# Kernel optimization log

Hardware: AMD Instinct MI355X
Metric: run time of the kernel (lower is better)

Reference implementation:

```python
import jax, jax.numpy as jnp
import numpy as np

B, S, H = 1, 2048, 2048
HD, NQ, NKV = 128, 16, 4
FFH = 8192
EPS = 1e-5
ROPE_BASE = 10000.0
SOFTMAX_CAP = 50.0
CLIP_L, CLIP_R = 0.0, 1.0


def setup_inputs() -> dict:
    key = jax.random.key(0)
    ks = jax.random.split(key, 10)
    std = 0.02
    return {
        "x": jax.random.normal(ks[0], (B, S, H), dtype=jnp.float32),
        "attn_norm_w": jax.random.uniform(ks[1], (H,), minval=-1.0, maxval=1.0, dtype=jnp.float32),
        "mlp_norm_w": jax.random.uniform(ks[2], (H,), minval=-1.0, maxval=1.0, dtype=jnp.float32),
        "wq": jax.random.normal(ks[3], (H, NQ * HD), dtype=jnp.float32) * std,
        "wk": jax.random.normal(ks[4], (H, NKV * HD), dtype=jnp.float32) * std,
        "wv": jax.random.normal(ks[5], (H, NKV * HD), dtype=jnp.float32) * std,
        "wo": jax.random.normal(ks[6], (NQ * HD, H), dtype=jnp.float32) * std,
        "w_gate": jax.random.normal(ks[7], (H, FFH), dtype=jnp.float32) * std,
        "w_up": jax.random.normal(ks[8], (H, FFH), dtype=jnp.float32) * std,
        "w_down": jax.random.normal(ks[9], (FFH, H), dtype=jnp.float32) * std,
    }


def _rms_norm(x, w):
    # GroupRMSNorm with group_size=None -> whole hidden dim
    var = jnp.mean(jnp.square(x), axis=-1, keepdims=True)
    return x * jax.lax.rsqrt(var + EPS) * w


def _rope_cos_sin(seq_len, dim):
    inv_freq = 1.0 / (ROPE_BASE ** (jnp.arange(0, dim, 2, dtype=jnp.float32) / dim))
    t = jnp.arange(seq_len, dtype=jnp.float32)
    freqs = jnp.outer(t, inv_freq)                      # [S, dim/2]
    emb = jnp.concatenate([freqs, freqs], axis=-1)      # [S, dim]
    return jnp.cos(emb), jnp.sin(emb)


def _apply_rope(x, cos, sin):
    # x: [B, S, h, d]; rotate-half (LLaMA-style)
    d = x.shape[-1]
    x1, x2 = x[..., : d // 2], x[..., d // 2 :]
    rot = jnp.concatenate([-x2, x1], axis=-1)
    return x * cos[None, :, None, :] + rot * sin[None, :, None, :]


def _qk_norm(x):
    # per-head RMS norm over head_dim (qk_norm_group_size == head_dim), unit weight
    var = jnp.mean(jnp.square(x), axis=-1, keepdims=True)
    return x * jax.lax.rsqrt(var + EPS)


def reference(x, attn_norm_w, mlp_norm_w, wq, wk, wv, wo, w_gate, w_up, w_down):
    # ---- attention sub-layer ----
    h = _rms_norm(x, attn_norm_w)                                     # [B,S,H]
    q = (h @ wq).reshape(B, S, NQ, HD)
    k = (h @ wk).reshape(B, S, NKV, HD)
    v = (h @ wv).reshape(B, S, NKV, HD)

    cos, sin = _rope_cos_sin(S, HD)
    q = _apply_rope(q, cos, sin)
    k = _apply_rope(k, cos, sin)

    q = _qk_norm(q)
    k = _qk_norm(k)

    # GQA: expand kv heads to match q heads
    rep = NQ // NKV
    k = jnp.repeat(k, rep, axis=2)                                    # [B,S,NQ,HD]
    v = jnp.repeat(v, rep, axis=2)

    scale = 1.0 / jnp.sqrt(jnp.float32(HD))
    scores = jnp.einsum("bshd,bthd->bhst", q, k) * scale              # [B,NQ,S,S]
    # softmax cap: cap * tanh(s / cap)
    scores = SOFTMAX_CAP * jnp.tanh(scores / SOFTMAX_CAP)
    causal = jnp.tril(jnp.ones((S, S), dtype=bool))
    scores = jnp.where(causal[None, None], scores, -jnp.inf)
    p = jax.nn.softmax(scores, axis=-1)
    # clip range (l, r): clamp(p * (r - l) + l, 0, 1)
    p = jnp.clip(p * (CLIP_R - CLIP_L) + CLIP_L, 0.0, 1.0)
    o = jnp.einsum("bhst,bthd->bshd", p, v).reshape(B, S, NQ * HD)
    x = x + o @ wo

    # ---- MLP sub-layer (gated SiLU) ----
    h2 = _rms_norm(x, mlp_norm_w)
    mlp_out = (jax.nn.silu(h2 @ w_gate) * (h2 @ w_up)) @ w_down
    return x + mlp_out
```

## Files before the change

### kernel.cpp

```cpp
#include <hip/hip_runtime.h>

typedef __bf16 bf16;
typedef __bf16 bf16x4 __attribute__((ext_vector_type(4)));
typedef __bf16 bf16x8 __attribute__((ext_vector_type(8)));
typedef float f32x4 __attribute__((ext_vector_type(4)));

#define GLP16(gp, lp) __builtin_amdgcn_global_load_lds( \
    (const __attribute__((address_space(1))) void*)(gp), \
    (__attribute__((address_space(3))) void*)(lp), 16, 0, 0)

__device__ __forceinline__ f32x4 mfma16(bf16x8 a, bf16x8 b, f32x4 c) {
    return __builtin_amdgcn_mfma_f32_16x16x32_bf16(a, b, c, 0, 0, 0);
}

__global__ __launch_bounds__(256) void k_rmsnorm(const float* __restrict__ x,
        const float* __restrict__ w, bf16* __restrict__ out) {
    const int H = 2048;
    size_t row = blockIdx.x;
    const float* xr = x + row * H;
    int base = threadIdx.x * 8;
    float4 a = *(const float4*)(xr + base);
    float4 b = *(const float4*)(xr + base + 4);
    float ss = a.x*a.x + a.y*a.y + a.z*a.z + a.w*a.w
             + b.x*b.x + b.y*b.y + b.z*b.z + b.w*b.w;
#pragma unroll
    for (int m = 32; m > 0; m >>= 1) ss += __shfl_xor(ss, m);
    __shared__ float red[4];
    if ((threadIdx.x & 63) == 0) red[threadIdx.x >> 6] = ss;
    __syncthreads();
    float tot = red[0] + red[1] + red[2] + red[3];
    float rs = rsqrtf(tot * (1.0f / H) + 1e-5f);
    float4 wa = *(const float4*)(w + base);
    float4 wb = *(const float4*)(w + base + 4);
    bf16x8 ov;
    ov[0] = (bf16)(a.x * rs * wa.x); ov[1] = (bf16)(a.y * rs * wa.y);
    ov[2] = (bf16)(a.z * rs * wa.z); ov[3] = (bf16)(a.w * rs * wa.w);
    ov[4] = (bf16)(b.x * rs * wb.x); ov[5] = (bf16)(b.y * rs * wb.y);
    ov[6] = (bf16)(b.z * rs * wb.z); ov[7] = (bf16)(b.w * rs * wb.w);
    *(bf16x8*)(out + row * H + base) = ov;
}

__global__ __launch_bounds__(256) void k_convT(const float* __restrict__ W,
        bf16* __restrict__ Wt, int K, int N, int rmul, int roff) {
    __shared__ float t[64][65];
    int k0 = blockIdx.x * 64, n0 = blockIdx.y * 64;
    int tid = threadIdx.x;
#pragma unroll
    for (int it = 0; it < 4; it++) {
        int idx = it * 256 + tid;
        int r = idx >> 4, c = (idx & 15) * 4;
        float4 v = *(const float4*)(W + (size_t)(k0 + r) * N + n0 + c);
        t[r][c] = v.x; t[r][c + 1] = v.y; t[r][c + 2] = v.z; t[r][c + 3] = v.w;
    }
    __syncthreads();
#pragma unroll
    for (int it = 0; it < 4; it++) {
        int idx = it * 256 + tid;
        int n = idx >> 4, kc = (idx & 15) * 4;
        bf16x4 o;
#pragma unroll
        for (int j = 0; j < 4; j++) o[j] = (bf16)t[kc + j][n];
        *(bf16x4*)(Wt + ((size_t)(n0 + n) * rmul + roff) * K + k0 + kc) = o;
    }
}

__global__ __launch_bounds__(256) void k_transpose(const bf16* __restrict__ in,
        bf16* __restrict__ out, int R, int C) {
    __shared__ bf16 t[32][33];
    int r0 = blockIdx.x * 32, c0 = blockIdx.y * 32;
    int tx = threadIdx.x & 31, ty = threadIdx.x >> 5;
#pragma unroll
    for (int i = 0; i < 4; i++)
        t[ty + i * 8][tx] = in[(size_t)(r0 + ty + i * 8) * C + c0 + tx];
    __syncthreads();
#pragma unroll
    for (int i = 0; i < 4; i++)
        out[(size_t)(c0 + ty + i * 8) * R + r0 + tx] = t[tx][ty + i * 8];
}

template<int EPI>
__global__ __launch_bounds__(512, 2) void k_gemm8(const bf16* __restrict__ A,
        const bf16* __restrict__ Bt, void* __restrict__ outp,
        const void* __restrict__ aux, int M, int N, int K, int ksplit) {
    extern __shared__ char lds[];
    const int tid = threadIdx.x, wave = tid >> 6, lane = tid & 63;
    const int lr = lane & 15, kg = lane >> 4;
    const int wm = wave >> 2, wn = wave & 3;
    const int bn = blockIdx.x, bm = blockIdx.y, split = blockIdx.z;
    const int row0 = bm * 256, col0 = bn * 256;
    const int kbeg = split * ksplit;
    const int NT = ksplit >> 6;
    const size_t K2 = (size_t)K * 2;
    const int xorm = (lr & 7) << 4;

    size_t soff[2];
#pragma unroll
    for (int s = 0; s < 2; s++) {
        int d = s * 8192 + tid * 16;
        int rh = d >> 7, c = d & 127;
        soff[s] = (size_t)rh * K2 + (c ^ ((rh & 7) << 4));
    }
    const char* Ab = (const char*)A + ((size_t)row0 * K + kbeg) * 2;
    const char* Bb = (const char*)Bt + ((size_t)col0 * K + kbeg) * 2;

    auto stA = [&](int t, int mh) {
        const char* src = Ab + (size_t)(mh * 128) * K2 + (size_t)t * 128;
        char* dst = lds + (t & 1) * 32768 + mh * 16384 + wave * 1024;
        GLP16(src + soff[0], dst);
        GLP16(src + soff[1], dst + 8192);
    };
    auto stB = [&](int t, int nh) {
        const char* src = Bb + (size_t)(nh * 128) * K2 + (size_t)t * 128;
        char* dst = lds + 65536 + (t & 1) * 32768 + nh * 16384 + wave * 1024;
        GLP16(src + soff[0], dst);
        GLP16(src + soff[1], dst + 8192);
    };

    f32x4 acc[8][4];
#pragma unroll
    for (int m = 0; m < 8; m++)
#pragma unroll
        for (int n = 0; n < 4; n++) acc[m][n] = (f32x4){0, 0, 0, 0};

    bf16x8 a[8], c0[4], c1[4];
    auto rdA = [&](const char* base, int mh) {
#pragma unroll
        for (int mi = 0; mi < 4; mi++)
#pragma unroll
            for (int kk = 0; kk < 2; kk++) {
                int rh = wm * 64 + mi * 16 + lr;
                int c = (kk * 64 + kg * 16) ^ xorm;
                a[mi * 2 + kk] = *(const bf16x8*)(base + mh * 16384 + rh * 128 + c);
            }
    };
    auto rdB = [&](const char* base, int nh, bf16x8 (&b)[4]) {
#pragma unroll
        for (int nj = 0; nj < 2; nj++)
#pragma unroll
            for (int kk = 0; kk < 2; kk++) {
                int rh = wn * 32 + nj * 16 + lr;
                int c = (kk * 64 + kg * 16) ^ xorm;
                b[nj * 2 + kk] = *(const bf16x8*)(base + nh * 16384 + rh * 128 + c);
            }
    };
    auto mm = [&](int mh, int nh, bf16x8 (&b)[4]) {
#pragma unroll
        for (int mi = 0; mi < 4; mi++)
#pragma unroll
            for (int nj = 0; nj < 2; nj++)
#pragma unroll
                for (int kk = 0; kk < 2; kk++)
                    acc[mh * 4 + mi][nh * 2 + nj] =
                        mfma16(a[mi * 2 + kk], b[nj * 2 + kk],
                               acc[mh * 4 + mi][nh * 2 + nj]);
    };

#define PBAR do { asm volatile("" ::: "memory"); \
                  __builtin_amdgcn_s_barrier(); \
                  asm volatile("" ::: "memory"); } while (0)

    stA(0, 0); stA(0, 1); stB(0, 0); stB(0, 1);
    asm volatile("s_waitcnt vmcnt(0)" ::: "memory");
    PBAR;

    for (int t = 0; t < NT; ++t) {
        const char* Ac = lds + (t & 1) * 32768;
        const char* Bc = lds + 65536 + (t & 1) * 32768;
        const bool m1 = (t + 1 < NT);
        rdA(Ac, 0); rdB(Bc, 0, c0); rdB(Bc, 1, c1);
        if (m1) { stA(t + 1, 0); stA(t + 1, 1); stB(t + 1, 0); stB(t + 1, 1); }
        __builtin_amdgcn_s_setprio(1);
        mm(0, 0, c0); mm(0, 1, c1);
        __builtin_amdgcn_s_setprio(0);
        PBAR;
        rdA(Ac, 1);
        __builtin_amdgcn_s_setprio(1);
        mm(1, 0, c0); mm(1, 1, c1);
        __builtin_amdgcn_s_setprio(0);
        if (m1) asm volatile("s_waitcnt vmcnt(0)" ::: "memory");
        PBAR;
    }
#undef PBAR

#pragma unroll
    for (int mi = 0; mi < 8; mi++)
#pragma unroll
        for (int ni = 0; ni < 4; ni++)
#pragma unroll
            for (int r = 0; r < 4; r++) {
                size_t row = row0 + (mi >> 2) * 128 + wm * 64 + (mi & 3) * 16 + kg * 4 + r;
                size_t col = col0 + (ni >> 1) * 128 + wn * 32 + (ni & 1) * 16 + lr;
                float vv = acc[mi][ni][r];
                if (EPI == 5) {
                    ((bf16*)outp)[(size_t)split * M * N + row * N + col] = (bf16)vv;
                } else {
                    float pv = __shfl_xor(vv, 1);
                    float g = (lane & 1) ? pv : vv;
                    float u = (lane & 1) ? vv : pv;
                    float sg = g / (1.0f + __expf(-g));
                    if (!(lane & 1))
                        ((bf16*)outp)[row * (size_t)(N >> 1) + (col >> 1)] =
                            (bf16)(sg * u);
                }
            }
}

__global__ __launch_bounds__(256) void k_reduce(const bf16* __restrict__ parts,
        const float* __restrict__ resid, float* __restrict__ out,
        int ns, size_t n8) {
    size_t i = (size_t)blockIdx.x * 256 + threadIdx.x;
    if (i >= n8) return;
    size_t base = i * 8;
    float4 a = *(const float4*)(resid + base);
    float4 b = *(const float4*)(resid + base + 4);
    for (int s = 0; s < ns; s++) {
        bf16x8 p = *(const bf16x8*)(parts + (size_t)s * n8 * 8 + base);
        a.x += (float)p[0]; a.y += (float)p[1]; a.z += (float)p[2]; a.w += (float)p[3];
        b.x += (float)p[4]; b.y += (float)p[5]; b.z += (float)p[6]; b.w += (float)p[7];
    }
    *(float4*)(out + base) = a;
    *(float4*)(out + base + 4) = b;
}

__global__ __launch_bounds__(256) void k_reduce_rms(const bf16* __restrict__ parts,
        const float* __restrict__ resid, const float* __restrict__ w,
        float* __restrict__ x2, bf16* __restrict__ hb, int ns) {
    const int H = 2048;
    size_t row = blockIdx.x;
    int base = threadIdx.x * 8;
    const float* rr = resid + row * H + base;
    float4 a = *(const float4*)rr;
    float4 b = *(const float4*)(rr + 4);
    for (int s = 0; s < ns; s++) {
        bf16x8 p = *(const bf16x8*)(parts + (size_t)s * H * 2048 + row * H + base);
        a.x += (float)p[0]; a.y += (float)p[1]; a.z += (float)p[2]; a.w += (float)p[3];
        b.x += (float)p[4]; b.y += (float)p[5]; b.z += (float)p[6]; b.w += (float)p[7];
    }
    *(float4*)(x2 + row * H + base) = a;
    *(float4*)(x2 + row * H + base + 4) = b;
    float ss = a.x*a.x + a.y*a.y + a.z*a.z + a.w*a.w
             + b.x*b.x + b.y*b.y + b.z*b.z + b.w*b.w;
#pragma unroll
    for (int m = 32; m > 0; m >>= 1) ss += __shfl_xor(ss, m);
    __shared__ float red[4];
    if ((threadIdx.x & 63) == 0) red[threadIdx.x >> 6] = ss;
    __syncthreads();
    float tot = red[0] + red[1] + red[2] + red[3];
    float rs = rsqrtf(tot * (1.0f / H) + 1e-5f);
    float4 wa = *(const float4*)(w + base);
    float4 wb = *(const float4*)(w + base + 4);
    bf16x8 ov;
    ov[0] = (bf16)(a.x * rs * wa.x); ov[1] = (bf16)(a.y * rs * wa.y);
    ov[2] = (bf16)(a.z * rs * wa.z); ov[3] = (bf16)(a.w * rs * wa.w);
    ov[4] = (bf16)(b.x * rs * wb.x); ov[5] = (bf16)(b.y * rs * wb.y);
    ov[6] = (bf16)(b.z * rs * wb.z); ov[7] = (bf16)(b.w * rs * wb.w);
    *(bf16x8*)(hb + row * H + base) = ov;
}

__global__ __launch_bounds__(256) void k_qkvrope(const bf16* __restrict__ parts,
        bf16* __restrict__ qb, bf16* __restrict__ kb, bf16* __restrict__ vb) {
    int s = blockIdx.x;
    int tid = threadIdx.x, wave = tid >> 6, lane = tid & 63;
    const bf16* p0 = parts + (size_t)s * 3072;
    const bf16* p1 = p0 + (size_t)2048 * 3072;
    float f = exp2f((float)lane * -0.2076205059304601f);
    float sn, cs;
    sincosf((float)s * f, &sn, &cs);
#pragma unroll 1
    for (int pass = 0; pass < 5; pass++) {
        int h = pass * 4 + wave;
        int base = (h < 16) ? h * 128 : 2048 + (h - 16) * 128;
        int c1 = base + lane, c2 = c1 + 64;
        float x1 = (float)p0[c1] + (float)p1[c1];
        float x2 = (float)p0[c2] + (float)p1[c2];
        float o1 = x1 * cs - x2 * sn;
        float o2 = x2 * cs + x1 * sn;
        float ss = o1 * o1 + o2 * o2;
#pragma unroll
        for (int m = 32; m > 0; m >>= 1) ss += __shfl_xor(ss, m);
        float rs = rsqrtf(ss * (1.0f / 128.0f) + 1e-5f);
        bf16* dst = (h < 16) ? (qb + (size_t)s * 2048 + h * 128)
                             : (kb + (size_t)s * 512 + (h - 16) * 128);
        dst[lane] = (bf16)(o1 * rs);
        dst[lane + 64] = (bf16)(o2 * rs);
    }
    int c = 2560 + tid * 2;
    float v0 = (float)p0[c] + (float)p1[c];
    float v1 = (float)p0[c + 1] + (float)p1[c + 1];
    bf16* vd = vb + (size_t)s * 512 + tid * 2;
    vd[0] = (bf16)v0; vd[1] = (bf16)v1;
}

__global__ __launch_bounds__(256, 2) void k_attn(const bf16* __restrict__ qg,
        const bf16* __restrict__ kgl, const bf16* __restrict__ vtg,
        bf16* __restrict__ og) {
    extern __shared__ char alds[];
    int pi = blockIdx.x, h = blockIdx.y, kvh = h >> 2;
    int qt = (pi & 1) ? (31 - (pi >> 1)) : (pi >> 1);
    int nt = qt + 1;
    int tid = threadIdx.x, wave = tid >> 6, lane = tid & 63;
    int lr = lane & 15, kgrp = lane >> 4;

    int rowQ[4], colQ[4], rowV[4], colV[4];
#pragma unroll
    for (int j = 0; j < 4; j++) {
        int p = j * 4096 + wave * 1024 + lane * 16;
        int ps = p ^ (((p >> 8) & 7) << 4);
        rowQ[j] = ps >> 8; colQ[j] = ps & 255;
        int pv = p ^ (((p >> 7) & 7) << 4);
        rowV[j] = pv >> 7; colV[j] = pv & 127;
    }

    const float C1 = 0.08838834764831845f / 50.0f;
    const float L2E50 = 72.13475204444817f;

#pragma unroll
    for (int j = 0; j < 4; j++)
        GLP16((const char*)qg + (size_t)(qt * 64 + rowQ[j]) * 4096 + h * 256 + colQ[j],
              alds + j * 4096 + wave * 1024);
    for (int t = 0; t < 2 && t < nt; t++) {
#pragma unroll
        for (int j = 0; j < 4; j++)
            GLP16((const char*)kgl + (size_t)(t * 64 + rowQ[j]) * 1024 + kvh * 256 + colQ[j],
                  alds + 16384 + t * 16384 + j * 4096 + wave * 1024);
#pragma unroll
        for (int j = 0; j < 4; j++)
            GLP16((const char*)vtg + (size_t)(kvh * 128 + rowV[j]) * 4096 + t * 128 + colV[j],
                  alds + 49152 + t * 16384 + j * 4096 + wave * 1024);
    }
    if (nt > 1) asm volatile("s_waitcnt vmcnt(8)" ::: "memory");
    else        asm volatile("s_waitcnt vmcnt(0)" ::: "memory");
    __builtin_amdgcn_s_barrier();

    bf16x8 qf[4];
#pragma unroll
    for (int c = 0; c < 4; c++) {
        int b = (wave * 16 + lr) * 256 + c * 64 + kgrp * 16;
        qf[c] = *(const bf16x8*)(alds + (b ^ (((b >> 8) & 7) << 4)));
    }
    __builtin_amdgcn_s_barrier();

    f32x4 accO[8];
#pragma unroll
    for (int n = 0; n < 8; n++) accO[n] = (f32x4){0, 0, 0, 0};
    float lsum[4] = {0, 0, 0, 0};
    int qrow = qt * 64 + wave * 16 + kgrp * 4;

    for (int kt = 0; kt < nt; kt++) {
        int buf = kt & 1;
        const char* Kb = alds + 16384 + buf * 16384;
        const char* Vb = alds + 49152 + buf * 16384;
        char* Pb = alds;
#pragma unroll
        for (int j = 0; j < 4; j++) {
            f32x4 s = {0, 0, 0, 0};
#pragma unroll
            for (int c = 0; c < 4; c++) {
                int b = (j * 16 + lr) * 256 + c * 64 + kgrp * 16;
                bf16x8 kf = *(const bf16x8*)(Kb + (b ^ (((b >> 8) & 7) << 4)));
                s = mfma16(qf[c], kf, s);
            }
            int key = kt * 64 + j * 16 + lr;
#pragma unroll
            for (int r = 0; r < 4; r++) {
                float y = s[r] * C1;
                float y2 = y * y;
                float u = fmaf(y2, 0.13333333f, -0.33333333f);
                u = fmaf(y2, u, 1.0f);
                float t5 = y * u;
                float pe = fmaf(t5, L2E50, -L2E50);
                float pv = (key <= qrow + r) ? exp2f(pe) : 0.0f;
                lsum[r] += pv;
                int wb = (wave * 16 + kgrp * 4 + r) * 128 + (j * 16 + lr) * 2;
                *(bf16*)(Pb + (wb ^ (((wb >> 7) & 7) << 4))) = (bf16)pv;
            }
        }
        bf16x8 pf[2];
#pragma unroll
        for (int ks2 = 0; ks2 < 2; ks2++) {
            int b = (wave * 16 + lr) * 128 + ks2 * 64 + kgrp * 16;
            pf[ks2] = *(const bf16x8*)(Pb + (b ^ (((b >> 7) & 7) << 4)));
        }
#pragma unroll
        for (int n = 0; n < 8; n++)
#pragma unroll
            for (int ks2 = 0; ks2 < 2; ks2++) {
                int b = (n * 16 + lr) * 128 + ks2 * 64 + kgrp * 16;
                bf16x8 vf = *(const bf16x8*)(Vb + (b ^ (((b >> 7) & 7) << 4)));
                accO[n] = mfma16(pf[ks2], vf, accO[n]);
            }
        __builtin_amdgcn_s_barrier();
        bool more = (kt + 2 < nt);
        if (more) {
            int t = kt + 2;
#pragma unroll
            for (int j = 0; j < 4; j++)
                GLP16((const char*)kgl + (size_t)(t * 64 + rowQ[j]) * 1024 + kvh * 256 + colQ[j],
                      alds + 16384 + buf * 16384 + j * 4096 + wave * 1024);
#pragma unroll
            for (int j = 0; j < 4; j++)
                GLP16((const char*)vtg + (size_t)(kvh * 128 + rowV[j]) * 4096 + t * 128 + colV[j],
                      alds + 49152 + buf * 16384 + j * 4096 + wave * 1024);
        }
        if (kt + 1 < nt) {
            if (more) asm volatile("s_waitcnt vmcnt(8)" ::: "memory");
            else      asm volatile("s_waitcnt vmcnt(0)" ::: "memory");
            __builtin_amdgcn_s_barrier();
        }
    }
#pragma unroll
    for (int r = 0; r < 4; r++) {
        float t = lsum[r];
        t += __shfl_xor(t, 1); t += __shfl_xor(t, 2);
        t += __shfl_xor(t, 4); t += __shfl_xor(t, 8);
        lsum[r] = t;
    }
#pragma unroll
    for (int n = 0; n < 8; n++)
#pragma unroll
        for (int r = 0; r < 4; r++) {
            size_t row = qt * 64 + wave * 16 + kgrp * 4 + r;
            og[row * 2048 + h * 128 + n * 16 + lr] = (bf16)(accO[n][r] / lsum[r]);
        }
}

extern "C" void kernel_launch(void* const* d_in, const int* in_sizes, int n_in,
                              void* d_out, int out_size, void* d_ws, size_t ws_size,
                              hipStream_t stream) {
    const float* x      = (const float*)d_in[0];
    const float* attn_w = (const float*)d_in[1];
    const float* mlp_w  = (const float*)d_in[2];
    const float* wq     = (const float*)d_in[3];
    const float* wk     = (const float*)d_in[4];
    const float* wv     = (const float*)d_in[5];
    const float* wo     = (const float*)d_in[6];
    const float* wgate  = (const float*)d_in[7];
    const float* wup    = (const float*)d_in[8];
    const float* wdown  = (const float*)d_in[9];
    float* out = (float*)d_out;
    char* ws = (char*)d_ws;

    const size_t MB = 1024 * 1024;
    bf16* Wqkv = (bf16*)(ws + 0);
    bf16* vt   = (bf16*)(ws + 0);
    bf16* pO   = (bf16*)(ws + 0);
    bf16* Wgu  = (bf16*)(ws + 0);
    bf16* pD   = (bf16*)(ws + 0);
    bf16* WoT  = (bf16*)(ws + 64 * MB);
    bf16* WdT  = (bf16*)(ws + 64 * MB);
    bf16* hb   = (bf16*)(ws + 96 * MB);
    bf16* qb   = (bf16*)(ws + 104 * MB);
    bf16* kb   = (bf16*)(ws + 112 * MB);
    bf16* vb   = (bf16*)(ws + 114 * MB);
    bf16* ob   = (bf16*)(ws + 116 * MB);
    float* x2  = (float*)(ws + 124 * MB);
    bf16* gb   = (bf16*)(ws + 140 * MB);
    bf16* pQ   = (bf16*)(ws + 172 * MB);

    const int LDS8 = 131072;
    hipFuncSetAttribute((const void*)&k_gemm8<4>,
        hipFuncAttributeMaxDynamicSharedMemorySize, LDS8);
    hipFuncSetAttribute((const void*)&k_gemm8<5>,
        hipFuncAttributeMaxDynamicSharedMemorySize, LDS8);
    const int LDSA = 81920;
    hipFuncSetAttribute((const void*)&k_attn,
        hipFuncAttributeMaxDynamicSharedMemorySize, LDSA);

    const size_t n8 = (size_t)2048 * 2048 / 8;

    k_rmsnorm<<<2048, 256, 0, stream>>>(x, attn_w, hb);
    k_convT<<<dim3(32, 32), 256, 0, stream>>>(wq, Wqkv, 2048, 2048, 1, 0);
    k_convT<<<dim3(32, 8), 256, 0, stream>>>(wk, Wqkv + 4194304, 2048, 512, 1, 0);
    k_convT<<<dim3(32, 8), 256, 0, stream>>>(wv, Wqkv + 5242880, 2048, 512, 1, 0);
    k_gemm8<5><<<dim3(12, 8, 2), 512, LDS8, stream>>>(hb, Wqkv, pQ, nullptr,
                                                      2048, 3072, 2048, 1024);
    k_qkvrope<<<2048, 256, 0, stream>>>(pQ, qb, kb, vb);
    k_transpose<<<dim3(64, 16), 256, 0, stream>>>(vb, vt, 2048, 512);
    k_attn<<<dim3(32, 16), 256, LDSA, stream>>>(qb, kb, vt, ob);
    k_convT<<<dim3(32, 32), 256, 0, stream>>>(wo, WoT, 2048, 2048, 1, 0);
    k_gemm8<5><<<dim3(8, 8, 4), 512, LDS8, stream>>>(ob, WoT, pO, nullptr,
                                                     2048, 2048, 2048, 512);
    k_reduce_rms<<<2048, 256, 0, stream>>>(pO, x, mlp_w, x2, hb, 4);
    k_convT<<<dim3(32, 128), 256, 0, stream>>>(wgate, Wgu, 2048, 8192, 2, 0);
    k_convT<<<dim3(32, 128), 256, 0, stream>>>(wup, Wgu, 2048, 8192, 2, 1);
    k_gemm8<4><<<dim3(64, 8, 1), 512, LDS8, stream>>>(hb, Wgu, gb, nullptr,
                                                      2048, 16384, 2048, 2048);
    k_convT<<<dim3(128, 32), 256, 0, stream>>>(wdown, WdT, 8192, 2048, 1, 0);
    k_gemm8<5><<<dim3(8, 8, 4), 512, LDS8, stream>>>(gb, WdT, pD, nullptr,
                                                     2048, 2048, 8192, 2048);
    k_reduce<<<2048, 256, 0, stream>>>(pD, x2, out, 4, n8);
}
```

Measured before the change: 438.2 us.

## Shrink GEMM tile to 256x128 with BK=32, two-stage prefetch, higher occupancy

Replaces the 256x256x64 GEMM with a 256x128 tile, K-step 32, and an 8-wave 4x2 layout in which each wave owns a 64x64 sub-tile. It prefetches two stages ahead using vmcnt-based waits. LDS use drops to 48KB and launch bounds now request 4 blocks per CU, with twice as many blocks in every GEMM launch. The aim is better latency hiding through occupancy and deeper prefetch, at the cost of less operand reuse per block and more barriers per unit of K.

Result: slower. 473.3 us (+8.0%).

```diff
diff --git a/kernel.cpp b/kernel.cpp
--- a/kernel.cpp
+++ b/kernel.cpp
@@ -79,118 +79,111 @@
 }
 
 template<int EPI>
-__global__ __launch_bounds__(512, 2) void k_gemm8(const bf16* __restrict__ A,
+__global__ __launch_bounds__(512, 4) void k_gemm9(const bf16* __restrict__ A,
         const bf16* __restrict__ Bt, void* __restrict__ outp,
         const void* __restrict__ aux, int M, int N, int K, int ksplit) {
     extern __shared__ char lds[];
     const int tid = threadIdx.x, wave = tid >> 6, lane = tid & 63;
     const int lr = lane & 15, kg = lane >> 4;
-    const int wm = wave >> 2, wn = wave & 3;
+    const int wm = wave >> 1, wn = wave & 1;
     const int bn = blockIdx.x, bm = blockIdx.y, split = blockIdx.z;
-    const int row0 = bm * 256, col0 = bn * 256;
+    const int row0 = bm * 256, col0 = bn * 128;
     const int kbeg = split * ksplit;
-    const int NT = ksplit >> 6;
+    const int NT = ksplit >> 5;
     const size_t K2 = (size_t)K * 2;
-    const int xorm = (lr & 7) << 4;
-
-    size_t soff[2];
-#pragma unroll
-    for (int s = 0; s < 2; s++) {
-        int d = s * 8192 + tid * 16;
-        int rh = d >> 7, c = d & 127;
-        soff[s] = (size_t)rh * K2 + (c ^ ((rh & 7) << 4));
+
+    int soffA[2], soffB;
+    {
+#pragma unroll
+        for (int s = 0; s < 2; s++) {
+            int d = wave * 2048 + s * 1024 + lane * 16;
+            int line = d >> 7, w = d & 127;
+            int wp = w ^ ((line & 7) << 4);
+            soffA[s] = (line * 2 + (wp >> 6)) * (int)K2 + (wp & 63);
+        }
+        int d = wave * 1024 + lane * 16;
+        int line = d >> 7, w = d & 127;
+        int wp = w ^ ((line & 7) << 4);
+        soffB = (line * 2 + (wp >> 6)) * (int)K2 + (wp & 63);
     }
     const char* Ab = (const char*)A + ((size_t)row0 * K + kbeg) * 2;
     const char* Bb = (const char*)Bt + ((size_t)col0 * K + kbeg) * 2;
 
-    auto stA = [&](int t, int mh) {
-        const char* src = Ab + (size_t)(mh * 128) * K2 + (size_t)t * 128;
-        char* dst = lds + (t & 1) * 32768 + mh * 16384 + wave * 1024;
-        GLP16(src + soff[0], dst);
-        GLP16(src + soff[1], dst + 8192);
+    auto stage = [&](int t) {
+        const char* sa = Ab + (size_t)t * 64;
+        char* da = lds + (t & 1) * 16384 + wave * 2048;
+        GLP16(sa + soffA[0], da);
+        GLP16(sa + soffA[1], da + 1024);
+        const char* sb = Bb + (size_t)t * 64;
+        char* db = lds + 32768 + (t & 1) * 8192 + wave * 1024;
+        GLP16(sb + soffB, db);
     };
-    auto stB = [&](int t, int nh) {
-        const char* src = Bb + (size_t)(nh * 128) * K2 + (size_t)t * 128;
-        char* dst = lds + 65536 + (t & 1) * 32768 + nh * 16384 + wave * 1024;
-        GLP16(src + soff[0], dst);
-        GLP16(src + soff[1], dst + 8192);
+
+    f32x4 acc[4][4];
+#pragma unroll
+    for (int m = 0; m < 4; m++)
+#pragma unroll
+        for (int n = 0; n < 4; n++) acc[m][n] = (f32x4){0, 0, 0, 0};
+
+    bf16x8 a[4], b[4];
+    auto rdA = [&](const char* base) {
+#pragma unroll
+        for (int mi = 0; mi < 4; mi++) {
+            int r = wm * 64 + mi * 16 + lr;
+            int line = r >> 1;
+            int off = (((r & 1) << 6) + (kg << 4)) ^ ((line & 7) << 4);
+            a[mi] = *(const bf16x8*)(base + line * 128 + off);
+        }
     };
-
-    f32x4 acc[8][4];
-#pragma unroll
-    for (int m = 0; m < 8; m++)
-#pragma unroll
-        for (int n = 0; n < 4; n++) acc[m][n] = (f32x4){0, 0, 0, 0};
-
-    bf16x8 a[8], c0[4], c1[4];
-    auto rdA = [&](const char* base, int mh) {
+    auto rdB = [&](const char* base) {
+#pragma unroll
+        for (int nj = 0; nj < 4; nj++) {
+            int r = wn * 64 + nj * 16 + lr;
+            int line = r >> 1;
+            int off = (((r & 1) << 6) + (kg << 4)) ^ ((line & 7) << 4);
+            b[nj] = *(const bf16x8*)(base + line * 128 + off);
+        }
+    };
+    auto mm2 = [&](int njb) {
 #pragma unroll
         for (int mi = 0; mi < 4; mi++)
 #pragma unroll
-            for (int kk = 0; kk < 2; kk++) {
-                int rh = wm * 64 + mi * 16 + lr;
-                int c = (kk * 64 + kg * 16) ^ xorm;
-                a[mi * 2 + kk] = *(const bf16x8*)(base + mh * 16384 + rh * 128 + c);
-            }
-    };
-    auto rdB = [&](const char* base, int nh, bf16x8 (&b)[4]) {
-#pragma unroll
-        for (int nj = 0; nj < 2; nj++)
-#pragma unroll
-            for (int kk = 0; kk < 2; kk++) {
-                int rh = wn * 32 + nj * 16 + lr;
-                int c = (kk * 64 + kg * 16) ^ xorm;
-                b[nj * 2 + kk] = *(const bf16x8*)(base + nh * 16384 + rh * 128 + c);
-            }
-    };
-    auto mm = [&](int mh, int nh, bf16x8 (&b)[4]) {
-#pragma unroll
-        for (int mi = 0; mi < 4; mi++)
-#pragma unroll
-            for (int nj = 0; nj < 2; nj++)
-#pragma unroll
-                for (int kk = 0; kk < 2; kk++)
-                    acc[mh * 4 + mi][nh * 2 + nj] =
-                        mfma16(a[mi * 2 + kk], b[nj * 2 + kk],
-                               acc[mh * 4 + mi][nh * 2 + nj]);
+            for (int dn = 0; dn < 2; dn++)
+                acc[mi][njb + dn] = mfma16(a[mi], b[njb + dn], acc[mi][njb + dn]);
     };
 
 #define PBAR do { asm volatile("" ::: "memory"); \
                   __builtin_amdgcn_s_barrier(); \
                   asm volatile("" ::: "memory"); } while (0)
 
-    stA(0, 0); stA(0, 1); stB(0, 0); stB(0, 1);
-    asm volatile("s_waitcnt vmcnt(0)" ::: "memory");
+    stage(0); stage(1);
+    asm volatile("s_waitcnt vmcnt(3)" ::: "memory");
     PBAR;
 
-    for (int t = 0; t < NT; ++t) {
-        const char* Ac = lds + (t & 1) * 32768;
-        const char* Bc = lds + 65536 + (t & 1) * 32768;
-        const bool m1 = (t + 1 < NT);
-        rdA(Ac, 0); rdB(Bc, 0, c0); rdB(Bc, 1, c1);
-        if (m1) { stA(t + 1, 0); stA(t + 1, 1); stB(t + 1, 0); stB(t + 1, 1); }
-        __builtin_amdgcn_s_setprio(1);
-        mm(0, 0, c0); mm(0, 1, c1);
-        __builtin_amdgcn_s_setprio(0);
+    for (int s = 0; s < NT; ++s) {
+        const char* Ac = lds + (s & 1) * 16384;
+        const char* Bc = lds + 32768 + (s & 1) * 8192;
+        rdA(Ac); rdB(Bc);
+        __builtin_amdgcn_s_setprio(1); mm2(0); __builtin_amdgcn_s_setprio(0);
+        asm volatile("s_waitcnt lgkmcnt(0)" ::: "memory");
         PBAR;
-        rdA(Ac, 1);
-        __builtin_amdgcn_s_setprio(1);
-        mm(1, 0, c0); mm(1, 1, c1);
-        __builtin_amdgcn_s_setprio(0);
-        if (m1) asm volatile("s_waitcnt vmcnt(0)" ::: "memory");
+        if (s + 2 < NT) stage(s + 2);
+        __builtin_amdgcn_s_setprio(1); mm2(2); __builtin_amdgcn_s_setprio(0);
+        if (s + 2 < NT)      asm volatile("s_waitcnt vmcnt(3)" ::: "memory");
+        else if (s + 1 < NT) asm volatile("s_waitcnt vmcnt(0)" ::: "memory");
         PBAR;
     }
 #undef PBAR
 
 #pragma unroll
-    for (int mi = 0; mi < 8; mi++)
-#pragma unroll
-        for (int ni = 0; ni < 4; ni++)
+    for (int mi = 0; mi < 4; mi++)
+#pragma unroll
+        for (int nj = 0; nj < 4; nj++)
 #pragma unroll
             for (int r = 0; r < 4; r++) {
-                size_t row = row0 + (mi >> 2) * 128 + wm * 64 + (mi & 3) * 16 + kg * 4 + r;
-                size_t col = col0 + (ni >> 1) * 128 + wn * 32 + (ni & 1) * 16 + lr;
-                float vv = acc[mi][ni][r];
+                size_t row = row0 + wm * 64 + mi * 16 + kg * 4 + r;
+                size_t col = col0 + wn * 64 + nj * 16 + lr;
+                float vv = acc[mi][nj][r];
                 if (EPI == 5) {
                     ((bf16*)outp)[(size_t)split * M * N + row * N + col] = (bf16)vv;
                 } else {
@@ -457,11 +450,11 @@
     bf16* gb   = (bf16*)(ws + 140 * MB);
     bf16* pQ   = (bf16*)(ws + 172 * MB);
 
-    const int LDS8 = 131072;
-    hipFuncSetAttribute((const void*)&k_gemm8<4>,
-        hipFuncAttributeMaxDynamicSharedMemorySize, LDS8);
-    hipFuncSetAttribute((const void*)&k_gemm8<5>,
-        hipFuncAttributeMaxDynamicSharedMemorySize, LDS8);
+    const int LDS9 = 49152;
+    hipFuncSetAttribute((const void*)&k_gemm9<4>,
+        hipFuncAttributeMaxDynamicSharedMemorySize, LDS9);
+    hipFuncSetAttribute((const void*)&k_gemm9<5>,
+        hipFuncAttributeMaxDynamicSharedMemorySize, LDS9);
     const int LDSA = 81920;
     hipFuncSetAttribute((const void*)&k_attn,
         hipFuncAttributeMaxDynamicSharedMemorySize, LDSA);
@@ -472,21 +465,21 @@
     k_convT<<<dim3(32, 32), 256, 0, stream>>>(wq, Wqkv, 2048, 2048, 1, 0);
     k_convT<<<dim3(32, 8), 256, 0, stream>>>(wk, Wqkv + 4194304, 2048, 512, 1, 0);
     k_convT<<<dim3(32, 8), 256, 0, stream>>>(wv, Wqkv + 5242880, 2048, 512, 1, 0);
-    k_gemm8<5><<<dim3(12, 8, 2), 512, LDS8, stream>>>(hb, Wqkv, pQ, nullptr,
+    k_gemm9<5><<<dim3(24, 8, 2), 512, LDS9, stream>>>(hb, Wqkv, pQ, nullptr,
                                                       2048, 3072, 2048, 1024);
     k_qkvrope<<<2048, 256, 0, stream>>>(pQ, qb, kb, vb);
     k_transpose<<<dim3(64, 16), 256, 0, stream>>>(vb, vt, 2048, 512);
     k_attn<<<dim3(32, 16), 256, LDSA, stream>>>(qb, kb, vt, ob);
     k_convT<<<dim3(32, 32), 256, 0, stream>>>(wo, WoT, 2048, 2048, 1, 0);
-    k_gemm8<5><<<dim3(8, 8, 4), 512, LDS8, stream>>>(ob, WoT, pO, nullptr,
-                                                     2048, 2048, 2048, 512);
+    k_gemm9<5><<<dim3(16, 8, 4), 512, LDS9, stream>>>(ob, WoT, pO, nullptr,
+                                                      2048, 2048, 2048, 512);
     k_reduce_rms<<<2048, 256, 0, stream>>>(pO, x, mlp_w, x2, hb, 4);
     k_convT<<<dim3(32, 128), 256, 0, stream>>>(wgate, Wgu, 2048, 8192, 2, 0);
     k_convT<<<dim3(32, 128), 256, 0, stream>>>(wup, Wgu, 2048, 8192, 2, 1);
-    k_gemm8<4><<<dim3(64, 8, 1), 512, LDS8, stream>>>(hb, Wgu, gb, nullptr,
-                                                      2048, 16384, 2048, 2048);
+    k_gemm9<4><<<dim3(128, 8, 1), 512, LDS9, stream>>>(hb, Wgu, gb, nullptr,
+                                                       2048, 16384, 2048, 2048);
     k_convT<<<dim3(128, 32), 256, 0, stream>>>(wdown, WdT, 8192, 2048, 1, 0);
-    k_gemm8<5><<<dim3(8, 8, 4), 512, LDS8, stream>>>(gb, WdT, pD, nullptr,
-                                                     2048, 2048, 8192, 2048);
+    k_gemm9<5><<<dim3(16, 8, 4), 512, LDS9, stream>>>(gb, WdT, pD, nullptr,
+                                                      2048, 2048, 8192, 2048);
     k_reduce<<<2048, 256, 0, stream>>>(pD, x2, out, 4, n8);
 }
```

## Switch GEMM inner loop to 32x32x16 MFMA with per-wave 128x64 tiles

Applied to the files above, without the earlier changes.

The GEMM kernel now uses 32x32x16 bf16 MFMA instructions instead of 16x16x32. Each wave computes a 128x64 sub-tile instead of two 64x32 halves, and the LDS read pattern, staging loop and epilogue index mapping are rewritten to match. The larger MFMA shape issues fewer instructions and does fewer LDS fragment reads per FLOP. In exchange, register pressure and accumulator layout change, and the epilogue's SiLU pairing now depends on the new lane-to-column mapping.

Result: slower. 463.1 us (+5.7%).

```diff
diff --git a/kernel.cpp b/kernel.cpp
--- a/kernel.cpp
+++ b/kernel.cpp
@@ -4,6 +4,7 @@
 typedef __bf16 bf16x4 __attribute__((ext_vector_type(4)));
 typedef __bf16 bf16x8 __attribute__((ext_vector_type(8)));
 typedef float f32x4 __attribute__((ext_vector_type(4)));
+typedef float f32x16 __attribute__((ext_vector_type(16)));
 
 #define GLP16(gp, lp) __builtin_amdgcn_global_load_lds( \
     (const __attribute__((address_space(1))) void*)(gp), \
@@ -11,6 +12,9 @@
 
 __device__ __forceinline__ f32x4 mfma16(bf16x8 a, bf16x8 b, f32x4 c) {
     return __builtin_amdgcn_mfma_f32_16x16x32_bf16(a, b, c, 0, 0, 0);
+}
+__device__ __forceinline__ f32x16 mfma32(bf16x8 a, bf16x8 b, f32x16 c) {
+    return __builtin_amdgcn_mfma_f32_32x32x16_bf16(a, b, c, 0, 0, 0);
 }
 
 __global__ __launch_bounds__(256) void k_rmsnorm(const float* __restrict__ x,
@@ -79,87 +83,76 @@
 }
 
 template<int EPI>
-__global__ __launch_bounds__(512, 2) void k_gemm8(const bf16* __restrict__ A,
+__global__ __launch_bounds__(512, 2) void k_gemm10(const bf16* __restrict__ A,
         const bf16* __restrict__ Bt, void* __restrict__ outp,
         const void* __restrict__ aux, int M, int N, int K, int ksplit) {
     extern __shared__ char lds[];
     const int tid = threadIdx.x, wave = tid >> 6, lane = tid & 63;
-    const int lr = lane & 15, kg = lane >> 4;
+    const int l31 = lane & 31, lh = lane >> 5;
     const int wm = wave >> 2, wn = wave & 3;
     const int bn = blockIdx.x, bm = blockIdx.y, split = blockIdx.z;
     const int row0 = bm * 256, col0 = bn * 256;
     const int kbeg = split * ksplit;
     const int NT = ksplit >> 6;
     const size_t K2 = (size_t)K * 2;
-    const int xorm = (lr & 7) << 4;
-
-    size_t soff[2];
-#pragma unroll
-    for (int s = 0; s < 2; s++) {
-        int d = s * 8192 + tid * 16;
-        int rh = d >> 7, c = d & 127;
-        soff[s] = (size_t)rh * K2 + (c ^ ((rh & 7) << 4));
+
+    int soff[4];
+#pragma unroll
+    for (int c = 0; c < 4; c++) {
+        int d = c * 8192 + tid * 16;
+        int rh = d >> 7, w = d & 127;
+        soff[c] = rh * (int)K2 + (w ^ ((rh & 7) << 4));
     }
     const char* Ab = (const char*)A + ((size_t)row0 * K + kbeg) * 2;
     const char* Bb = (const char*)Bt + ((size_t)col0 * K + kbeg) * 2;
 
-    auto stA = [&](int t, int mh) {
-        const char* src = Ab + (size_t)(mh * 128) * K2 + (size_t)t * 128;
-        char* dst = lds + (t & 1) * 32768 + mh * 16384 + wave * 1024;
-        GLP16(src + soff[0], dst);
-        GLP16(src + soff[1], dst + 8192);
+    auto stage = [&](int t) {
+        const char* sa = Ab + (size_t)t * 128;
+        char* da = lds + (t & 1) * 32768 + wave * 1024;
+        const char* sb = Bb + (size_t)t * 128;
+        char* db = lds + 65536 + (t & 1) * 32768 + wave * 1024;
+#pragma unroll
+        for (int c = 0; c < 4; c++) {
+            GLP16(sa + soff[c], da + c * 8192);
+            GLP16(sb + soff[c], db + c * 8192);
+        }
     };
-    auto stB = [&](int t, int nh) {
-        const char* src = Bb + (size_t)(nh * 128) * K2 + (size_t)t * 128;
-        char* dst = lds + 65536 + (t & 1) * 32768 + nh * 16384 + wave * 1024;
-        GLP16(src + soff[0], dst);
-        GLP16(src + soff[1], dst + 8192);
+
+    f32x16 acc[4][2];
+#pragma unroll
+    for (int m = 0; m < 4; m++)
+#pragma unroll
+        for (int n = 0; n < 2; n++) acc[m][n] = (f32x16)(0.0f);
+
+    bf16x8 a0[4], a1[4], b0[4], b1[4];
+    auto rdA = [&](const char* base, int mb, bf16x8 (&arr)[4]) {
+        int line = wm * 128 + mb * 32 + l31;
+        const char* p = base + line * 128;
+        int xr = (line & 7) << 4;
+#pragma unroll
+        for (int ks = 0; ks < 4; ks++)
+            arr[ks] = *(const bf16x8*)(p + ((ks * 32 + lh * 16) ^ xr));
     };
-
-    f32x4 acc[8][4];
-#pragma unroll
-    for (int m = 0; m < 8; m++)
-#pragma unroll
-        for (int n = 0; n < 4; n++) acc[m][n] = (f32x4){0, 0, 0, 0};
-
-    bf16x8 a[8], c0[4], c1[4];
-    auto rdA = [&](const char* base, int mh) {
-#pragma unroll
-        for (int mi = 0; mi < 4; mi++)
-#pragma unroll
-            for (int kk = 0; kk < 2; kk++) {
-                int rh = wm * 64 + mi * 16 + lr;
-                int c = (kk * 64 + kg * 16) ^ xorm;
-                a[mi * 2 + kk] = *(const bf16x8*)(base + mh * 16384 + rh * 128 + c);
-            }
+    auto rdB = [&](const char* base, int nb, bf16x8 (&arr)[4]) {
+        int line = wn * 64 + nb * 32 + l31;
+        const char* p = base + line * 128;
+        int xr = (line & 7) << 4;
+#pragma unroll
+        for (int ks = 0; ks < 4; ks++)
+            arr[ks] = *(const bf16x8*)(p + ((ks * 32 + lh * 16) ^ xr));
     };
-    auto rdB = [&](const char* base, int nh, bf16x8 (&b)[4]) {
-#pragma unroll
-        for (int nj = 0; nj < 2; nj++)
-#pragma unroll
-            for (int kk = 0; kk < 2; kk++) {
-                int rh = wn * 32 + nj * 16 + lr;
-                int c = (kk * 64 + kg * 16) ^ xorm;
-                b[nj * 2 + kk] = *(const bf16x8*)(base + nh * 16384 + rh * 128 + c);
-            }
-    };
-    auto mm = [&](int mh, int nh, bf16x8 (&b)[4]) {
-#pragma unroll
-        for (int mi = 0; mi < 4; mi++)
-#pragma unroll
-            for (int nj = 0; nj < 2; nj++)
-#pragma unroll
-                for (int kk = 0; kk < 2; kk++)
-                    acc[mh * 4 + mi][nh * 2 + nj] =
-                        mfma16(a[mi * 2 + kk], b[nj * 2 + kk],
-                               acc[mh * 4 + mi][nh * 2 + nj]);
+    auto mm = [&](int mb, bf16x8 (&af)[4]) {
+#pragma unroll
+        for (int ks = 0; ks < 4; ks++) acc[mb][0] = mfma32(af[ks], b0[ks], acc[mb][0]);
+#pragma unroll
+        for (int ks = 0; ks < 4; ks++) acc[mb][1] = mfma32(af[ks], b1[ks], acc[mb][1]);
     };
 
 #define PBAR do { asm volatile("" ::: "memory"); \
                   __builtin_amdgcn_s_barrier(); \
                   asm volatile("" ::: "memory"); } while (0)
 
-    stA(0, 0); stA(0, 1); stB(0, 0); stB(0, 1);
+    stage(0);
     asm volatile("s_waitcnt vmcnt(0)" ::: "memory");
     PBAR;
 
@@ -167,15 +160,15 @@
         const char* Ac = lds + (t & 1) * 32768;
         const char* Bc = lds + 65536 + (t & 1) * 32768;
         const bool m1 = (t + 1 < NT);
-        rdA(Ac, 0); rdB(Bc, 0, c0); rdB(Bc, 1, c1);
-        if (m1) { stA(t + 1, 0); stA(t + 1, 1); stB(t + 1, 0); stB(t + 1, 1); }
+        rdA(Ac, 0, a0); rdA(Ac, 1, a1); rdB(Bc, 0, b0); rdB(Bc, 1, b1);
+        if (m1) stage(t + 1);
         __builtin_amdgcn_s_setprio(1);
-        mm(0, 0, c0); mm(0, 1, c1);
+        mm(0, a0); mm(1, a1);
         __builtin_amdgcn_s_setprio(0);
         PBAR;
-        rdA(Ac, 1);
+        rdA(Ac, 2, a0); rdA(Ac, 3, a1);
         __builtin_amdgcn_s_setprio(1);
-        mm(1, 0, c0); mm(1, 1, c1);
+        mm(2, a0); mm(3, a1);
         __builtin_amdgcn_s_setprio(0);
         if (m1) asm volatile("s_waitcnt vmcnt(0)" ::: "memory");
         PBAR;
@@ -183,26 +176,28 @@
 #undef PBAR
 
 #pragma unroll
-    for (int mi = 0; mi < 8; mi++)
-#pragma unroll
-        for (int ni = 0; ni < 4; ni++)
-#pragma unroll
-            for (int r = 0; r < 4; r++) {
-                size_t row = row0 + (mi >> 2) * 128 + wm * 64 + (mi & 3) * 16 + kg * 4 + r;
-                size_t col = col0 + (ni >> 1) * 128 + wn * 32 + (ni & 1) * 16 + lr;
-                float vv = acc[mi][ni][r];
-                if (EPI == 5) {
-                    ((bf16*)outp)[(size_t)split * M * N + row * N + col] = (bf16)vv;
-                } else {
-                    float pv = __shfl_xor(vv, 1);
-                    float g = (lane & 1) ? pv : vv;
-                    float u = (lane & 1) ? vv : pv;
-                    float sg = g / (1.0f + __expf(-g));
-                    if (!(lane & 1))
-                        ((bf16*)outp)[row * (size_t)(N >> 1) + (col >> 1)] =
-                            (bf16)(sg * u);
+    for (int mb = 0; mb < 4; mb++)
+#pragma unroll
+        for (int nb = 0; nb < 2; nb++)
+#pragma unroll
+            for (int g = 0; g < 4; g++)
+#pragma unroll
+                for (int r = 0; r < 4; r++) {
+                    size_t row = row0 + wm * 128 + mb * 32 + r + 8 * g + 4 * lh;
+                    size_t col = col0 + wn * 64 + nb * 32 + l31;
+                    float vv = acc[mb][nb][g * 4 + r];
+                    if (EPI == 5) {
+                        ((bf16*)outp)[(size_t)split * M * N + row * N + col] = (bf16)vv;
+                    } else {
+                        float pv = __shfl_xor(vv, 1);
+                        float g2 = (lane & 1) ? pv : vv;
+                        float u = (lane & 1) ? vv : pv;
+                        float sg = g2 / (1.0f + __expf(-g2));
+                        if (!(lane & 1))
+                            ((bf16*)outp)[row * (size_t)(N >> 1) + (col >> 1)] =
+                                (bf16)(sg * u);
+                    }
                 }
-            }
 }
 
 __global__ __launch_bounds__(256) void k_reduce(const bf16* __restrict__ parts,
@@ -457,11 +452,11 @@
     bf16* gb   = (bf16*)(ws + 140 * MB);
     bf16* pQ   = (bf16*)(ws + 172 * MB);
 
-    const int LDS8 = 131072;
-    hipFuncSetAttribute((const void*)&k_gemm8<4>,
-        hipFuncAttributeMaxDynamicSharedMemorySize, LDS8);
-    hipFuncSetAttribute((const void*)&k_gemm8<5>,
-        hipFuncAttributeMaxDynamicSharedMemorySize, LDS8);
+    const int LDS10 = 131072;
+    hipFuncSetAttribute((const void*)&k_gemm10<4>,
+        hipFuncAttributeMaxDynamicSharedMemorySize, LDS10);
+    hipFuncSetAttribute((const void*)&k_gemm10<5>,
+        hipFuncAttributeMaxDynamicSharedMemorySize, LDS10);
     const int LDSA = 81920;
     hipFuncSetAttribute((const void*)&k_attn,
         hipFuncAttributeMaxDynamicSharedMemorySize, LDSA);
@@ -472,21 +467,21 @@
     k_convT<<<dim3(32, 32), 256, 0, stream>>>(wq, Wqkv, 2048, 2048, 1, 0);
     k_convT<<<dim3(32, 8), 256, 0, stream>>>(wk, Wqkv + 4194304, 2048, 512, 1, 0);
     k_convT<<<dim3(32, 8), 256, 0, stream>>>(wv, Wqkv + 5242880, 2048, 512, 1, 0);
-    k_gemm8<5><<<dim3(12, 8, 2), 512, LDS8, stream>>>(hb, Wqkv, pQ, nullptr,
-                                                      2048, 3072, 2048, 1024);
+    k_gemm10<5><<<dim3(12, 8, 2), 512, LDS10, stream>>>(hb, Wqkv, pQ, nullptr,
+                                                        2048, 3072, 2048, 1024);
     k_qkvrope<<<2048, 256, 0, stream>>>(pQ, qb, kb, vb);
     k_transpose<<<dim3(64, 16), 256, 0, stream>>>(vb, vt, 2048, 512);
     k_attn<<<dim3(32, 16), 256, LDSA, stream>>>(qb, kb, vt, ob);
     k_convT<<<dim3(32, 32), 256, 0, stream>>>(wo, WoT, 2048, 2048, 1, 0);
-    k_gemm8<5><<<dim3(8, 8, 4), 512, LDS8, stream>>>(ob, WoT, pO, nullptr,
-                                                     2048, 2048, 2048, 512);
+    k_gemm10<5><<<dim3(8, 8, 4), 512, LDS10, stream>>>(ob, WoT, pO, nullptr,
+                                                       2048, 2048, 2048, 512);
     k_reduce_rms<<<2048, 256, 0, stream>>>(pO, x, mlp_w, x2, hb, 4);
     k_convT<<<dim3(32, 128), 256, 0, stream>>>(wgate, Wgu, 2048, 8192, 2, 0);
     k_convT<<<dim3(32, 128), 256, 0, stream>>>(wup, Wgu, 2048, 8192, 2, 1);
-    k_gemm8<4><<<dim3(64, 8, 1), 512, LDS8, stream>>>(hb, Wgu, gb, nullptr,
-                                                      2048, 16384, 2048, 2048);
+    k_gemm10<4><<<dim3(64, 8, 1), 512, LDS10, stream>>>(hb, Wgu, gb, nullptr,
+                                                        2048, 16384, 2048, 2048);
     k_convT<<<dim3(128, 32), 256, 0, stream>>>(wdown, WdT, 8192, 2048, 1, 0);
-    k_gemm8<5><<<dim3(8, 8, 4), 512, LDS8, stream>>>(gb, WdT, pD, nullptr,
-                                                     2048, 2048, 8192, 2048);
+    k_gemm10<5><<<dim3(8, 8, 4), 512, LDS10, stream>>>(gb, WdT, pD, nullptr,
+                                                       2048, 2048, 8192, 2048);
     k_reduce<<<2048, 256, 0, stream>>>(pD, x2, out, 4, n8);
 }
```

## Software-pipeline GEMM main loop to overlap LDS reads with MFMA across half-steps

Applied to the files above, without the earlier changes.

The GEMM main loop is restructured so the second-half MFMAs of tile t run in the next phase, interleaved with the LDS reads of tile t+1. Separate A-fragment registers (lo/hi) and ping-pong B-fragment buffers let LDS loads and matrix ops overlap across barriers instead of serialising within each half-step. This raises register pressure (extra fragment arrays) under a 512-thread, 2-block launch bound, which could cause spills or lower occupancy. The kernel is also renamed, with all launch sites updated.

Measured after the change: 884.0 us. 2.02x slower.

```diff
diff --git a/kernel.cpp b/kernel.cpp
--- a/kernel.cpp
+++ b/kernel.cpp
@@ -79,7 +79,7 @@
 }
 
 template<int EPI>
-__global__ __launch_bounds__(512, 2) void k_gemm8(const bf16* __restrict__ A,
+__global__ __launch_bounds__(512, 2) void k_gemm12(const bf16* __restrict__ A,
         const bf16* __restrict__ Bt, void* __restrict__ outp,
         const void* __restrict__ aux, int M, int N, int K, int ksplit) {
     extern __shared__ char lds[];
@@ -115,6 +115,9 @@
         GLP16(src + soff[0], dst);
         GLP16(src + soff[1], dst + 8192);
     };
+    auto stage = [&](int t) {
+        stA(t, 0); stA(t, 1); stB(t, 0); stB(t, 1);
+    };
 
     f32x4 acc[8][4];
 #pragma unroll
@@ -122,15 +125,15 @@
 #pragma unroll
         for (int n = 0; n < 4; n++) acc[m][n] = (f32x4){0, 0, 0, 0};
 
-    bf16x8 a[8], c0[4], c1[4];
-    auto rdA = [&](const char* base, int mh) {
+    bf16x8 aLo[8], aHi[8], cA0[4], cA1[4], cB0[4], cB1[4];
+    auto rdA = [&](const char* base, int mh, bf16x8 (&arr)[8]) {
 #pragma unroll
         for (int mi = 0; mi < 4; mi++)
 #pragma unroll
             for (int kk = 0; kk < 2; kk++) {
                 int rh = wm * 64 + mi * 16 + lr;
                 int c = (kk * 64 + kg * 16) ^ xorm;
-                a[mi * 2 + kk] = *(const bf16x8*)(base + mh * 16384 + rh * 128 + c);
+                arr[mi * 2 + kk] = *(const bf16x8*)(base + mh * 16384 + rh * 128 + c);
             }
     };
     auto rdB = [&](const char* base, int nh, bf16x8 (&b)[4]) {
@@ -143,7 +146,7 @@
                 b[nj * 2 + kk] = *(const bf16x8*)(base + nh * 16384 + rh * 128 + c);
             }
     };
-    auto mm = [&](int mh, int nh, bf16x8 (&b)[4]) {
+    auto mmf = [&](bf16x8 (&af)[8], int mh, int nh, bf16x8 (&b)[4]) {
 #pragma unroll
         for (int mi = 0; mi < 4; mi++)
 #pragma unroll
@@ -151,7 +154,7 @@
 #pragma unroll
                 for (int kk = 0; kk < 2; kk++)
                     acc[mh * 4 + mi][nh * 2 + nj] =
-                        mfma16(a[mi * 2 + kk], b[nj * 2 + kk],
+                        mfma16(af[mi * 2 + kk], b[nj * 2 + kk],
                                acc[mh * 4 + mi][nh * 2 + nj]);
     };
 
@@ -159,27 +162,46 @@
                   __builtin_amdgcn_s_barrier(); \
                   asm volatile("" ::: "memory"); } while (0)
 
-    stA(0, 0); stA(0, 1); stB(0, 0); stB(0, 1);
+    auto phaseA = [&](int t, bf16x8 (&CUR0)[4], bf16x8 (&CUR1)[4],
+                      bf16x8 (&PRV0)[4], bf16x8 (&PRV1)[4], bool domm) {
+        const char* Ac = lds + (t & 1) * 32768;
+        const char* Bc = lds + 65536 + (t & 1) * 32768;
+        rdA(Ac, 0, aLo); rdB(Bc, 0, CUR0); rdB(Bc, 1, CUR1);
+        if (domm) {
+            __builtin_amdgcn_s_setprio(1);
+            mmf(aHi, 1, 0, PRV0); mmf(aHi, 1, 1, PRV1);
+            __builtin_amdgcn_s_setprio(0);
+        }
+        if (t + 1 < NT) stage(t + 1);
+        PBAR;
+    };
+    auto phaseB = [&](int t, bf16x8 (&CUR0)[4], bf16x8 (&CUR1)[4]) {
+        const char* Ac = lds + (t & 1) * 32768;
+        rdA(Ac, 1, aHi);
+        __builtin_amdgcn_s_setprio(1);
+        mmf(aLo, 0, 0, CUR0); mmf(aLo, 0, 1, CUR1);
+        __builtin_amdgcn_s_setprio(0);
+        if (t + 1 < NT) asm volatile("s_waitcnt vmcnt(0)" ::: "memory");
+        PBAR;
+    };
+
+    stage(0);
     asm volatile("s_waitcnt vmcnt(0)" ::: "memory");
     PBAR;
-
-    for (int t = 0; t < NT; ++t) {
-        const char* Ac = lds + (t & 1) * 32768;
-        const char* Bc = lds + 65536 + (t & 1) * 32768;
-        const bool m1 = (t + 1 < NT);
-        rdA(Ac, 0); rdB(Bc, 0, c0); rdB(Bc, 1, c1);
-        if (m1) { stA(t + 1, 0); stA(t + 1, 1); stB(t + 1, 0); stB(t + 1, 1); }
-        __builtin_amdgcn_s_setprio(1);
-        mm(0, 0, c0); mm(0, 1, c1);
-        __builtin_amdgcn_s_setprio(0);
-        PBAR;
-        rdA(Ac, 1);
-        __builtin_amdgcn_s_setprio(1);
-        mm(1, 0, c0); mm(1, 1, c1);
-        __builtin_amdgcn_s_setprio(0);
-        if (m1) asm volatile("s_waitcnt vmcnt(0)" ::: "memory");
-        PBAR;
-    }
+    phaseA(0, cA0, cA1, cB0, cB1, false);
+    phaseB(0, cA0, cA1);
+
+    for (int tp = 1; tp + 1 < NT; tp += 2) {
+        phaseA(tp, cB0, cB1, cA0, cA1, true);
+        phaseB(tp, cB0, cB1);
+        phaseA(tp + 1, cA0, cA1, cB0, cB1, true);
+        phaseB(tp + 1, cA0, cA1);
+    }
+    phaseA(NT - 1, cB0, cB1, cA0, cA1, true);
+    phaseB(NT - 1, cB0, cB1);
+    __builtin_amdgcn_s_setprio(1);
+    mmf(aHi, 1, 0, cB0); mmf(aHi, 1, 1, cB1);
+    __builtin_amdgcn_s_setprio(0);
 #undef PBAR
 
 #pragma unroll
@@ -457,11 +479,11 @@
     bf16* gb   = (bf16*)(ws + 140 * MB);
     bf16* pQ   = (bf16*)(ws + 172 * MB);
 
-    const int LDS8 = 131072;
-    hipFuncSetAttribute((const void*)&k_gemm8<4>,
-        hipFuncAttributeMaxDynamicSharedMemorySize, LDS8);
-    hipFuncSetAttribute((const void*)&k_gemm8<5>,
-        hipFuncAttributeMaxDynamicSharedMemorySize, LDS8);
+    const int LDSG = 131072;
+    hipFuncSetAttribute((const void*)&k_gemm12<4>,
+        hipFuncAttributeMaxDynamicSharedMemorySize, LDSG);
+    hipFuncSetAttribute((const void*)&k_gemm12<5>,
+        hipFuncAttributeMaxDynamicSharedMemorySize, LDSG);
     const int LDSA = 81920;
     hipFuncSetAttribute((const void*)&k_attn,
         hipFuncAttributeMaxDynamicSharedMemorySize, LDSA);
@@ -472,21 +494,21 @@
     k_convT<<<dim3(32, 32), 256, 0, stream>>>(wq, Wqkv, 2048, 2048, 1, 0);
     k_convT<<<dim3(32, 8), 256, 0, stream>>>(wk, Wqkv + 4194304, 2048, 512, 1, 0);
     k_convT<<<dim3(32, 8), 256, 0, stream>>>(wv, Wqkv + 5242880, 2048, 512, 1, 0);
-    k_gemm8<5><<<dim3(12, 8, 2), 512, LDS8, stream>>>(hb, Wqkv, pQ, nullptr,
-                                                      2048, 3072, 2048, 1024);
+    k_gemm12<5><<<dim3(12, 8, 2), 512, LDSG, stream>>>(hb, Wqkv, pQ, nullptr,
+                                                       2048, 3072, 2048, 1024);
     k_qkvrope<<<2048, 256, 0, stream>>>(pQ, qb, kb, vb);
     k_transpose<<<dim3(64, 16), 256, 0, stream>>>(vb, vt, 2048, 512);
     k_attn<<<dim3(32, 16), 256, LDSA, stream>>>(qb, kb, vt, ob);
     k_convT<<<dim3(32, 32), 256, 0, stream>>>(wo, WoT, 2048, 2048, 1, 0);
-    k_gemm8<5><<<dim3(8, 8, 4), 512, LDS8, stream>>>(ob, WoT, pO, nullptr,
-                                                     2048, 2048, 2048, 512);
+    k_gemm12<5><<<dim3(8, 8, 4), 512, LDSG, stream>>>(ob, WoT, pO, nullptr,
+                                                      2048, 2048, 2048, 512);
     k_reduce_rms<<<2048, 256, 0, stream>>>(pO, x, mlp_w, x2, hb, 4);
     k_convT<<<dim3(32, 128), 256, 0, stream>>>(wgate, Wgu, 2048, 8192, 2, 0);
     k_convT<<<dim3(32, 128), 256, 0, stream>>>(wup, Wgu, 2048, 8192, 2, 1);
-    k_gemm8<4><<<dim3(64, 8, 1), 512, LDS8, stream>>>(hb, Wgu, gb, nullptr,
-                                                      2048, 16384, 2048, 2048);
+    k_gemm12<4><<<dim3(64, 8, 1), 512, LDSG, stream>>>(hb, Wgu, gb, nullptr,
+                                                       2048, 16384, 2048, 2048);
     k_convT<<<dim3(128, 32), 256, 0, stream>>>(wdown, WdT, 8192, 2048, 1, 0);
-    k_gemm8<5><<<dim3(8, 8, 4), 512, LDS8, stream>>>(gb, WdT, pD, nullptr,
-                                                     2048, 2048, 8192, 2048);
+    k_gemm12<5><<<dim3(8, 8, 4), 512, LDSG, stream>>>(gb, WdT, pD, nullptr,
+                                                      2048, 2048, 8192, 2048);
     k_reduce<<<2048, 256, 0, stream>>>(pD, x2, out, 4, n8);
 }
```
